# Optimization experiments

Measured on AMD Instinct MI355X. Metric: run time of the kernel, lower is better.

Reference implementation:

```python
import jax, jax.numpy as jnp
import numpy as np


def to_tb(r, size, base=4):
    # (B, size, size, size) -> (B, (size//base)^3, base, base, base)
    n = size // base
    r = r.reshape(-1, size, size, n, base)
    r = r.transpose(0, 1, 3, 2, 4)
    r = r.reshape(-1, size, n * n, base, base)
    r = r.transpose(0, 2, 1, 3, 4)
    return r.reshape(-1, n ** 3, base, base, base)


def from_tb(r, size, base=4):
    # inverse-ish of to_tb, ends with an extra (0,1,3,2) transpose as in source
    n = size // base
    r = r.reshape(-1, n * n, size, base, base)
    r = r.transpose(0, 2, 1, 3, 4)
    r = r.reshape(-1, size, size, n, base)
    r = r.transpose(0, 1, 3, 2, 4)
    r = r.reshape(-1, size, size, size)
    return r.transpose(0, 1, 3, 2)


def downscale(r, size):
    r = to_tb(r, size)  # base=4
    r = r.sum(axis=(2, 3, 4)) / 64.0
    r = r.reshape(-1, size // 4, size // 4, size // 4)
    return r.transpose(0, 3, 2, 1)


def setup_inputs() -> dict:
    key = jax.random.key(0)
    # (batch=2, level=4, 4, 4, 4^(3*4-2)) with 4*4*1048576 = 256^3 per slice
    x = jax.random.normal(key, (2, 4, 4, 4, 1048576), dtype=jnp.float32)
    return {"x": x}


def reference(x):
    level = x.shape[1]
    xt = jnp.transpose(x, (1, 0, 2, 3, 4))  # (level, batch, 4, 4, ...)
    batch = xt.shape[1]
    d2 = xt.shape[2]
    size_full = 4 ** level
    n3 = (4 ** (level - 1)) ** 3
    ret = []
    for i in range(level):
        r = xt[i]
        r = from_tb(r, size_full, 4 ** i)  # -> (batch, size, size, size)
        for k in range(i):
            r = downscale(r, 4 ** (level - k))
        for _ in range(i):
            r = jnp.tile(r, (1, 4, 4, 4))
        r = to_tb(r, size_full)  # (batch, n3, 4, 4, 4)
        ret.append(r.reshape(-1, n3, 64))
    out = jnp.stack(ret)  # (level, batch, n3, 64)
    out = out.transpose(1, 0, 2, 3).reshape(batch, -1, d2 ** 3)
    return out
```

## Files before the change

### kernel.cpp

```cpp
#include <hip/hip_runtime.h>


typedef float f4 __attribute__((ext_vector_type(4)));

__global__ __launch_bounds__(256) void k_reduce(const float* __restrict__ in,
                                                float* __restrict__ d1,
                                                float* __restrict__ p2,
                                                float* __restrict__ p3) {
    const int b = blockIdx.y;
    const int bx = blockIdx.x;
    const int tid = threadIdx.x;
    __shared__ float red[64];
    const f4* in4 = (const f4*)in;

    if (bx < 1024) {
        const int tlow = bx;
        const long base4 = (long)b * 16777216 + 4194304;
        float acc[4] = {0.f, 0.f, 0.f, 0.f};
        for (int dz = 0; dz < 4; ++dz) {
            long rb = base4 + (long)(dz * 1024 + tlow) * 1024;
#pragma unroll
            for (int k = 0; k < 4; ++k) {
                f4 v = __builtin_nontemporal_load(&in4[rb + k * 256 + tid]);
                acc[k] += v.x + v.y + v.z + v.w;
            }
        }
#pragma unroll
        for (int k = 0; k < 4; ++k) {
            acc[k] += __shfl_xor(acc[k], 4);
            acc[k] += __shfl_xor(acc[k], 8);
        }
        if ((tid & 12) == 0) {
            int yp = tlow >> 4;
            int zp = ((tlow & 15) << 2) + (tid & 3);
#pragma unroll
            for (int k = 0; k < 4; ++k) {
                int xp = k * 16 + (tid >> 4);
                int f4i = (zp >> 2) * 4096 + (yp >> 2) * 256 +
                          (xp >> 2) * 16 + (xp & 3) * 4 + (yp & 3);
                d1[b * 262144 + f4i * 4 + (zp & 3)] = acc[k] * (1.0f / 64.0f);
            }
        }
    } else if (bx < 2048) {
        const int blk = bx - 1024;
        const int g = blk & 3, cell = blk >> 2;
        const int yp = cell >> 4, xp = cell & 15;
        const long base4 = (long)b * 16777216 + 2 * 4194304 + yp * 16384 + xp * 1024;
        float acc = 0.f;
        for (int dzi = 0; dzi < 4; ++dzi) {
            long rb = base4 + (long)(g * 4 + dzi) * 262144;
#pragma unroll
            for (int k = 0; k < 4; ++k) {
                f4 v = __builtin_nontemporal_load(&in4[rb + k * 256 + tid]);
                acc += v.x + v.y + v.z + v.w;
            }
        }
        acc += __shfl_xor(acc, 1);
        acc += __shfl_xor(acc, 2);
        if ((tid & 3) == 0) red[tid >> 2] = acc;
        __syncthreads();
        if (tid < 16) {
            float s = red[tid] + red[16 + tid] + red[32 + tid] + red[48 + tid];
            p2[(b * 4 + g) * 4096 + xp * 256 + yp * 16 + tid] = s;
        }
    } else {
        const int blk = bx - 2048;
        const int kc = blk & 3;
        const int orig = blk >> 2;
        const int xp = orig >> 6, hi = (orig >> 2) & 15, dxg = orig & 3;
        const long base4 = (long)b * 16777216 + 3 * 4194304 +
                           (long)hi * 262144 + xp * 65536 + dxg * 16384;
        float acc = 0.f;
        for (int kk = 0; kk < 16; ++kk) {
            f4 v = __builtin_nontemporal_load(&in4[base4 + (kc * 16 + kk) * 256 + tid]);
            acc += v.x + v.y + v.z + v.w;
        }
        acc += __shfl_xor(acc, 1);
        acc += __shfl_xor(acc, 2);
        acc += __shfl_xor(acc, 4);
        acc += __shfl_xor(acc, 8);
        if ((tid & 15) == 0) red[tid >> 4] = acc;
        __syncthreads();
        if (tid < 16) {
            int G = (hi * 4 + dxg) * 4 + kc;
            p3[((b * 4 + xp) * 256 + G) * 16 + tid] = red[tid];
        }
    }
}

__global__ __launch_bounds__(256) void k_permcomb(const float* __restrict__ in,
                                                  float* __restrict__ out,
                                                  const float* __restrict__ p2,
                                                  const float* __restrict__ p3,
                                                  float* __restrict__ d2,
                                                  float* __restrict__ d3) {
    const int bx = blockIdx.x;
    const int tid = threadIdx.x;
    __shared__ float smem[16 * 260];

    if (bx < 8192) {
        const int b = bx >> 12;
        const int rem = bx & 4095;
        const int Y_hi = rem >> 6, Z_hi = rem & 63;
        const f4* in4 = (const f4*)in;
        f4* out4 = (f4*)out;
        const long in_b4 = (long)b * 16777216;
#pragma unroll
        for (int k = 0; k < 4; ++k) {
            int idx = k * 256 + tid;
            int r = idx >> 6;
            int col4 = idx & 63;
            int Y = Y_hi * 4 + (r >> 2), Z = Z_hi * 4 + (r & 3);
            f4 v = __builtin_nontemporal_load(&in4[in_b4 + (long)Y * 16384 + Z * 64 + col4]);
            *(f4*)&smem[r * 260 + col4 * 4] = v;
        }
        __syncthreads();
        const long out_b4 = (long)b * 16777216 + (long)Z_hi * 65536 + Y_hi * 1024;
#pragma unroll
        for (int k = 0; k < 4; ++k) {
            int idx = k * 256 + tid;
            int X = ((idx >> 4) << 2) + ((tid >> 2) & 3);
            int row0 = (tid & 3) * 4;
            f4 v;
            v.x = smem[(row0 + 0) * 260 + X];
            v.y = smem[(row0 + 1) * 260 + X];
            v.z = smem[(row0 + 2) * 260 + X];
            v.w = smem[(row0 + 3) * 260 + X];
            __builtin_nontemporal_store(v, &out4[out_b4 + idx]);
        }
    } else if (bx < 8224) {
        int idx = (bx - 8192) * 256 + tid;
        int b = idx >> 12, r = idx & 4095;
        int xp = r >> 8, yp = (r >> 4) & 15, zp = r & 15;
        float s = 0.f;
#pragma unroll
        for (int g = 0; g < 4; ++g) s += p2[(b * 4 + g) * 4096 + r];
        int f4i = (zp >> 2) * 256 + (yp >> 2) * 64 + (xp >> 2) * 16 + (xp & 3) * 4 + (yp & 3);
        d2[b * 4096 + f4i * 4 + (zp & 3)] = s * (1.0f / 4096.0f);
    } else {
        int v = bx - 8224;
        int b = v >> 2, xp = v & 3;
        int c = tid & 15, gp = tid >> 4;
        const float* pb = p3 + (long)((b * 4 + xp) * 256) * 16 + c;
        float s = 0.f;
#pragma unroll
        for (int j = 0; j < 16; ++j) s += pb[(gp * 16 + j) * 16];
        float* red = smem;
        red[gp * 16 + c] = s;
        __syncthreads();
        if (tid < 16) {
            float t = 0.f;
#pragma unroll
            for (int g = 0; g < 16; ++g) t += red[g * 16 + tid];
            d3[b * 64 + xp * 16 + tid] = t * (1.0f / 262144.0f);
        }
    }
}

__global__ __launch_bounds__(256) void k_bcast(const float* __restrict__ d1,
                                               const float* __restrict__ d2,
                                               const float* __restrict__ d3,
                                               float* __restrict__ out) {
    const int b = blockIdx.y;
    const int bx = blockIdx.x;
    const int tid = threadIdx.x;
    f4* out4 = (f4*)out;

    if (bx < 2048) {
        const f4* d14 = (const f4*)d1;
        const int bx0 = bx * 2;
        const int base = b * 65536 + ((bx0 >> 6) & 15) * 4096 + (bx0 & 15) * 256 + tid;
        const f4 v0 = d14[base];
        const f4 v1 = d14[base + 256];
        const long ob = (long)b * 16777216 + 4194304 + (long)bx * 2048;
#pragma unroll
        for (int j = 0; j < 8; ++j)
            __builtin_nontemporal_store((j < 4) ? v0 : v1, &out4[ob + j * 256 + tid]);
    } else if (bx < 4096) {
        const int blk = bx - 2048;
        const f4* d24 = (const f4*)d2;
        const int bx0 = blk * 2;
        const int base = b * 1024 + ((bx0 >> 6) & 3) * 256 + (bx0 & 3) * 64 + (tid & 63);
        const f4 v0 = d24[base];
        const f4 v1 = d24[base + 64];
        const long ob = (long)b * 16777216 + 2 * 4194304 + (long)blk * 2048;
#pragma unroll
        for (int j = 0; j < 8; ++j)
            __builtin_nontemporal_store((j < 4) ? v0 : v1, &out4[ob + j * 256 + tid]);
    } else {
        const int blk = bx - 4096;
        const f4* d34 = (const f4*)d3;
        const f4 v = d34[b * 16 + (tid & 15)];
        const long ob = (long)b * 16777216 + 3 * 4194304 + (long)blk * 2048;
#pragma unroll
        for (int j = 0; j < 8; ++j)
            __builtin_nontemporal_store(v, &out4[ob + j * 256 + tid]);
    }
}

extern "C" void kernel_launch(void* const* d_in, const int* in_sizes, int n_in,
                              void* d_out, int out_size, void* d_ws, size_t ws_size,
                              hipStream_t stream) {
    const float* in = (const float*)d_in[0];
    float* out = (float*)d_out;
    float* ws = (float*)d_ws;
    float* d1 = ws;
    float* p2 = ws + 524288;
    float* p3 = ws + 524288 + 65536;
    float* d2 = ws + 524288 + 65536 + 65536;
    float* d3 = ws + 524288 + 65536 + 65536 + 8192;
    k_reduce  <<<dim3(3072, 2), 256, 0, stream>>>(in, d1, p2, p3);
    k_permcomb<<<dim3(8232),    256, 0, stream>>>(in, out, p2, p3, d2, d3);
    k_bcast   <<<dim3(6144, 2), 256, 0, stream>>>(d1, d2, d3, out);
}
```

Measured before the change: 181.4 us.

## Fuse permute, final reductions and broadcast into one write kernel

Merges the permute kernel and the broadcast kernel into a single launch. Each broadcast block now combines the level-2 and level-3 partial sums on the fly, so the separate d2/d3 finalize step and its workspace round trip go away. This drops one kernel launch and one dependency barrier. In exchange, the level-2 and level-3 partials are re-read redundantly by many blocks, and the level-3 blocks repeat the small reduction in each block.

Result: slower. 186.6 us (+2.8%).

```diff
diff --git a/kernel.cpp b/kernel.cpp
--- a/kernel.cpp
+++ b/kernel.cpp
@@ -88,28 +88,26 @@
     }
 }
 
-__global__ __launch_bounds__(256) void k_permcomb(const float* __restrict__ in,
-                                                  float* __restrict__ out,
-                                                  const float* __restrict__ p2,
-                                                  const float* __restrict__ p3,
-                                                  float* __restrict__ d2,
-                                                  float* __restrict__ d3) {
+__global__ __launch_bounds__(256) void k_write(const float* __restrict__ in,
+                                               const float* __restrict__ d1,
+                                               const float* __restrict__ p2,
+                                               const float* __restrict__ p3,
+                                               float* __restrict__ out) {
+    const int b = blockIdx.y;
     const int bx = blockIdx.x;
     const int tid = threadIdx.x;
-    __shared__ float smem[16 * 260];
-
-    if (bx < 8192) {
-        const int b = bx >> 12;
-        const int rem = bx & 4095;
-        const int Y_hi = rem >> 6, Z_hi = rem & 63;
+    __shared__ f4 smem4[1040];
+    f4* out4 = (f4*)out;
+
+    if (bx < 4096) {
+        float* smem = (float*)smem4;
         const f4* in4 = (const f4*)in;
-        f4* out4 = (f4*)out;
+        const int Y_hi = bx >> 6, Z_hi = bx & 63;
         const long in_b4 = (long)b * 16777216;
 #pragma unroll
         for (int k = 0; k < 4; ++k) {
             int idx = k * 256 + tid;
-            int r = idx >> 6;
-            int col4 = idx & 63;
+            int r = idx >> 6, col4 = idx & 63;
             int Y = Y_hi * 4 + (r >> 2), Z = Z_hi * 4 + (r & 3);
             f4 v = __builtin_nontemporal_load(&in4[in_b4 + (long)Y * 16384 + Z * 64 + col4]);
             *(f4*)&smem[r * 260 + col4 * 4] = v;
@@ -128,72 +126,67 @@
             v.w = smem[(row0 + 3) * 260 + X];
             __builtin_nontemporal_store(v, &out4[out_b4 + idx]);
         }
-    } else if (bx < 8224) {
-        int idx = (bx - 8192) * 256 + tid;
-        int b = idx >> 12, r = idx & 4095;
-        int xp = r >> 8, yp = (r >> 4) & 15, zp = r & 15;
-        float s = 0.f;
-#pragma unroll
-        for (int g = 0; g < 4; ++g) s += p2[(b * 4 + g) * 4096 + r];
-        int f4i = (zp >> 2) * 256 + (yp >> 2) * 64 + (xp >> 2) * 16 + (xp & 3) * 4 + (yp & 3);
-        d2[b * 4096 + f4i * 4 + (zp & 3)] = s * (1.0f / 4096.0f);
-    } else {
-        int v = bx - 8224;
-        int b = v >> 2, xp = v & 3;
-        int c = tid & 15, gp = tid >> 4;
-        const float* pb = p3 + (long)((b * 4 + xp) * 256) * 16 + c;
-        float s = 0.f;
-#pragma unroll
-        for (int j = 0; j < 16; ++j) s += pb[(gp * 16 + j) * 16];
-        float* red = smem;
-        red[gp * 16 + c] = s;
-        __syncthreads();
-        if (tid < 16) {
-            float t = 0.f;
-#pragma unroll
-            for (int g = 0; g < 16; ++g) t += red[g * 16 + tid];
-            d3[b * 64 + xp * 16 + tid] = t * (1.0f / 262144.0f);
-        }
-    }
-}
-
-__global__ __launch_bounds__(256) void k_bcast(const float* __restrict__ d1,
-                                               const float* __restrict__ d2,
-                                               const float* __restrict__ d3,
-                                               float* __restrict__ out) {
-    const int b = blockIdx.y;
-    const int bx = blockIdx.x;
-    const int tid = threadIdx.x;
-    f4* out4 = (f4*)out;
-
-    if (bx < 2048) {
+    } else if (bx < 6144) {
+        const int blk = bx - 4096;
         const f4* d14 = (const f4*)d1;
-        const int bx0 = bx * 2;
+        const int bx0 = blk * 2;
         const int base = b * 65536 + ((bx0 >> 6) & 15) * 4096 + (bx0 & 15) * 256 + tid;
         const f4 v0 = d14[base];
         const f4 v1 = d14[base + 256];
-        const long ob = (long)b * 16777216 + 4194304 + (long)bx * 2048;
+        const long ob = (long)b * 16777216 + 4194304 + (long)blk * 2048;
 #pragma unroll
         for (int j = 0; j < 8; ++j)
             __builtin_nontemporal_store((j < 4) ? v0 : v1, &out4[ob + j * 256 + tid]);
-    } else if (bx < 4096) {
-        const int blk = bx - 2048;
-        const f4* d24 = (const f4*)d2;
+    } else if (bx < 8192) {
+        const int blk = bx - 6144;
+        const f4* p24 = (const f4*)p2;
         const int bx0 = blk * 2;
-        const int base = b * 1024 + ((bx0 >> 6) & 3) * 256 + (bx0 & 3) * 64 + (tid & 63);
-        const f4 v0 = d24[base];
-        const f4 v1 = d24[base + 64];
+        const int t6 = tid & 63;
+        const int xp = ((t6 >> 4) << 2) + ((t6 >> 2) & 3);
+        const int ylo = t6 & 3;
+        f4 v01[2];
+#pragma unroll
+        for (int r = 0; r < 2; ++r) {
+            int row = bx0 + r;
+            int zq = (row >> 6) & 3, yq = row & 3;
+            int yp = yq * 4 + ylo;
+            f4 s = {0.f, 0.f, 0.f, 0.f};
+#pragma unroll
+            for (int g = 0; g < 4; ++g)
+                s += p24[(b * 4 + g) * 1024 + xp * 64 + yp * 4 + zq];
+            v01[r] = s * (1.0f / 4096.0f);
+        }
         const long ob = (long)b * 16777216 + 2 * 4194304 + (long)blk * 2048;
 #pragma unroll
         for (int j = 0; j < 8; ++j)
-            __builtin_nontemporal_store((j < 4) ? v0 : v1, &out4[ob + j * 256 + tid]);
+            __builtin_nontemporal_store((j < 4) ? v01[0] : v01[1],
+                                        &out4[ob + j * 256 + tid]);
     } else {
-        const int blk = bx - 4096;
-        const f4* d34 = (const f4*)d3;
-        const f4 v = d34[b * 16 + (tid & 15)];
-        const long ob = (long)b * 16777216 + 3 * 4194304 + (long)blk * 2048;
-#pragma unroll
-        for (int j = 0; j < 8; ++j)
+        const int blk = bx - 8192;
+        const f4* p34 = (const f4*)p3;
+        const int o = tid & 15, part = tid >> 4;
+        const int xp = o >> 2, cq = o & 3;
+        f4 s = {0.f, 0.f, 0.f, 0.f};
+#pragma unroll
+        for (int j = 0; j < 16; ++j) {
+            int G = part * 16 + j;
+            s += p34[((b * 4 + xp) * 256 + G) * 4 + cq];
+        }
+        f4* red = smem4;
+        red[part * 16 + o] = s;
+        __syncthreads();
+        f4* tab = smem4 + 256;
+        if (tid < 16) {
+            f4 t = {0.f, 0.f, 0.f, 0.f};
+#pragma unroll
+            for (int g = 0; g < 16; ++g) t += red[g * 16 + tid];
+            tab[tid] = t * (1.0f / 262144.0f);
+        }
+        __syncthreads();
+        const f4 v = tab[tid & 15];
+        const long ob = (long)b * 16777216 + 3 * 4194304 + (long)blk * 8192;
+#pragma unroll
+        for (int j = 0; j < 32; ++j)
             __builtin_nontemporal_store(v, &out4[ob + j * 256 + tid]);
     }
 }
@@ -207,9 +200,6 @@
     float* d1 = ws;
     float* p2 = ws + 524288;
     float* p3 = ws + 524288 + 65536;
-    float* d2 = ws + 524288 + 65536 + 65536;
-    float* d3 = ws + 524288 + 65536 + 65536 + 8192;
-    k_reduce  <<<dim3(3072, 2), 256, 0, stream>>>(in, d1, p2, p3);
-    k_permcomb<<<dim3(8232),    256, 0, stream>>>(in, out, p2, p3, d2, d3);
-    k_bcast   <<<dim3(6144, 2), 256, 0, stream>>>(d1, d2, d3, out);
+    k_reduce<<<dim3(3072, 2), 256, 0, stream>>>(in, d1, p2, p3);
+    k_write <<<dim3(8704, 2), 256, 0, stream>>>(in, d1, p2, p3, out);
 }
```
